# Kernel tuning notes

Hardware: AMD Instinct MI355X
Metric: run time of the kernel (lower is better)

The kernel has to match this reference:

```python
import jax, jax.numpy as jnp
import numpy as np

ALPHA = 1.702   # GLU sigmoid scale
LIMIT = 7.0     # clamp limit
K = 2           # experts per token


def setup_inputs() -> dict:
    key = jax.random.key(0)
    ks = jax.random.split(key, 4)
    B, S, H, E, I = 1, 1024, 1024, 8, 1024
    return {
        "hidden_states": jax.random.normal(ks[0], (B, S, H), jnp.float32),
        "router_weight": jax.random.normal(ks[1], (E, H), jnp.float32),
        "router_bias": jnp.zeros((E,), jnp.float32),
        "gate_up_proj": jax.random.normal(ks[2], (E, H, 2 * I), jnp.float32) * 0.02,
        "gate_up_bias": jnp.zeros((E, 2 * I), jnp.float32),
        "down_proj": jax.random.normal(ks[3], (E, I, H), jnp.float32) * 0.02,
        "down_bias": jnp.zeros((E, H), jnp.float32),
    }


def reference(hidden_states, router_weight, router_bias, gate_up_proj,
              gate_up_bias, down_proj, down_bias):
    B, S, H = hidden_states.shape
    E = router_weight.shape[0]
    I = down_proj.shape[1]
    T = B * S

    flat = hidden_states.reshape(T, H)

    # Router: softmax over experts, top-K selection (weights NOT renormalized).
    logits = flat @ router_weight.T + router_bias               # [T, E]
    scores = jax.nn.softmax(logits, axis=-1)
    topk_vals, topk_idx = jax.lax.top_k(scores, K)              # [T, K]

    # Dense per-token expert weight matrix (equivalent of dispatch metadata +
    # combine * topk_weights in the tt pipeline); top-k indices are unique.
    w = jnp.zeros((T, E), scores.dtype).at[
        jnp.arange(T)[:, None], topk_idx].set(topk_vals)        # [T, E]

    # Expert MLP with clamped GLU (gpt-oss style).
    gu = jnp.einsum('th,ehf->tef', flat, gate_up_proj) + gate_up_bias  # [T,E,2I]
    gate = jnp.minimum(gu[..., :I], LIMIT)
    up = jnp.clip(gu[..., I:], -LIMIT, LIMIT)
    glu = gate * jax.nn.sigmoid(gate * ALPHA)
    act = (up + 1.0) * glu                                       # [T, E, I]

    down = jnp.einsum('tei,eih->teh', act, down_proj) + down_bias  # [T, E, H]

    # Weighted combine over selected experts.
    out = jnp.einsum('teh,te->th', down, w)
    return out.reshape(B, S, H)
```

## Files before the change

kernel.cpp:

```cpp
#include <hip/hip_runtime.h>
#include <hip/hip_bf16.h>


typedef unsigned short u16;
typedef __attribute__((ext_vector_type(8))) __bf16 bf16x8;
typedef __attribute__((ext_vector_type(4))) float f32x4;
typedef __attribute__((ext_vector_type(16))) float f32x16;

#define T_TOK 1024
#define H_DIM 1024
#define E_NUM 8
#define I_DIM 1024
#define ALPHA 1.702f
#define LIMIT 7.0f

__device__ __forceinline__ u16 f2bf(float f) {
    unsigned u = __builtin_bit_cast(unsigned, f);
    u = (u + 0x7FFFu + ((u >> 16) & 1u)) >> 16;
    return (u16)u;
}

__device__ __forceinline__ unsigned pk2(float lo, float hi) {
#if defined(__has_builtin) && __has_builtin(__builtin_amdgcn_cvt_pk_bf16_f32)
    typedef __attribute__((ext_vector_type(2))) __bf16 bf16x2_t;
    bf16x2_t v = __builtin_amdgcn_cvt_pk_bf16_f32(lo, hi);
    return __builtin_bit_cast(unsigned, v);
#else
    return (unsigned)f2bf(lo) | ((unsigned)f2bf(hi) << 16);
#endif
}

__device__ __forceinline__ f32x16 mfma32(bf16x8 a, bf16x8 b, f32x16 c) {
    return __builtin_amdgcn_mfma_f32_32x32x16_bf16(a, b, c, 0, 0, 0);
}

__device__ __forceinline__ void gld16(const void* g, void* l) {
    __builtin_amdgcn_global_load_lds(
        (const __attribute__((address_space(1))) void*)g,
        (__attribute__((address_space(3))) void*)l, 16, 0, 0);
}

__device__ __forceinline__ void expert_range(const int* counts, int e,
                                             int& cnt, int& abase) {
    int a = 0, c = 0;
#pragma unroll
    for (int i = 0; i < E_NUM; ++i) {
        int v = counts[i];
        if (i < e) a += v;
        if (i == e) c = v;
    }
    cnt = c; abase = a;
}

__global__ __launch_bounds__(256) void k_cvt(
    const float* __restrict__ gup, const float* __restrict__ dp,
    u16* __restrict__ gupT, u16* __restrict__ dpT, int* __restrict__ counts)
{
    if (blockIdx.x == 0 && threadIdx.x < E_NUM) counts[threadIdx.x] = 0;
    const int b = blockIdx.x;
    const float* src; u16* dst; int C, k0, c0;
    if (b < 4096) {
        int e = b >> 9, t = b & 511;
        k0 = (t >> 5) * 64; c0 = (t & 31) * 64;
        src = gup + ((size_t)e << 21); dst = gupT + ((size_t)e << 21); C = 2048;
    } else {
        int b2 = b - 4096;
        int e = b2 >> 8, t = b2 & 255;
        k0 = (t >> 4) * 64; c0 = (t & 15) * 64;
        src = dp + ((size_t)e << 20); dst = dpT + ((size_t)e << 20); C = 1024;
    }
    __shared__ __align__(16) u16 Ls[64][72];
    const int tid = threadIdx.x;
    const int kq = tid >> 4, cq = tid & 15;
    float4 v0 = *(const float4*)(src + (size_t)(k0 + kq * 4 + 0) * C + c0 + cq * 4);
    float4 v1 = *(const float4*)(src + (size_t)(k0 + kq * 4 + 1) * C + c0 + cq * 4);
    float4 v2 = *(const float4*)(src + (size_t)(k0 + kq * 4 + 2) * C + c0 + cq * 4);
    float4 v3 = *(const float4*)(src + (size_t)(k0 + kq * 4 + 3) * C + c0 + cq * 4);
    const float* p0 = (const float*)&v0; const float* p1 = (const float*)&v1;
    const float* p2 = (const float*)&v2; const float* p3 = (const float*)&v3;
#pragma unroll
    for (int i = 0; i < 4; ++i) {
        *(uint2*)&Ls[cq * 4 + i][kq * 4] =
            make_uint2(pk2(p0[i], p1[i]), pk2(p2[i], p3[i]));
    }
    __syncthreads();
    const int oc = tid >> 2, och = (tid & 3) * 16;
    u16* orow = dst + (size_t)(c0 + oc) * 1024 + k0 + och;
    *(uint4*)(orow)     = *(uint4*)&Ls[oc][och];
    *(uint4*)(orow + 8) = *(uint4*)&Ls[oc][och + 8];
}

__global__ __launch_bounds__(256) void k_router(
    const float* __restrict__ x, const float* __restrict__ rw,
    const float* __restrict__ rb, const float* __restrict__ db,
    int* __restrict__ counts, int* __restrict__ tok_list,
    float* __restrict__ w_list, u16* __restrict__ xb,
    float* __restrict__ out)
{
    const int t = blockIdx.x;
    const int tid = threadIdx.x;
    const float4 xv = *(const float4*)(x + (size_t)t * H_DIM + tid * 4);

    *(uint2*)(xb + (size_t)t * H_DIM + tid * 4) =
        make_uint2(pk2(xv.x, xv.y), pk2(xv.z, xv.w));

    float p[E_NUM];
#pragma unroll
    for (int e = 0; e < E_NUM; ++e) {
        const float4 wv = *(const float4*)(rw + e * H_DIM + tid * 4);
        p[e] = xv.x * wv.x + xv.y * wv.y + xv.z * wv.z + xv.w * wv.w;
    }
#pragma unroll
    for (int off = 32; off; off >>= 1) {
#pragma unroll
        for (int e = 0; e < E_NUM; ++e) p[e] += __shfl_down(p[e], off, 64);
    }
    __shared__ float red[4][E_NUM];
    __shared__ int se[2];
    __shared__ float sw[2];
    const int lane = tid & 63, wvid = tid >> 6;
    if (lane == 0) {
#pragma unroll
        for (int e = 0; e < E_NUM; ++e) red[wvid][e] = p[e];
    }
    __syncthreads();
    if (tid == 0) {
        float lg[E_NUM];
#pragma unroll
        for (int e = 0; e < E_NUM; ++e)
            lg[e] = red[0][e] + red[1][e] + red[2][e] + red[3][e] + rb[e];
        float m1 = -1e30f, m2 = -1e30f; int i1 = 0, i2 = 0;
#pragma unroll
        for (int e = 0; e < E_NUM; ++e) {
            float l = lg[e];
            if (l > m1) { m2 = m1; i2 = i1; m1 = l; i1 = e; }
            else if (l > m2) { m2 = l; i2 = e; }
        }
        float s = 0.f;
#pragma unroll
        for (int e = 0; e < E_NUM; ++e) s += __expf(lg[e] - m1);
        const float w0 = 1.0f / s;
        const float w1 = __expf(m2 - m1) / s;
        int slot0 = atomicAdd(&counts[i1], 1);
        tok_list[i1 * T_TOK + slot0] = t;
        w_list[i1 * T_TOK + slot0] = w0;
        int slot1 = atomicAdd(&counts[i2], 1);
        tok_list[i2 * T_TOK + slot1] = t;
        w_list[i2 * T_TOK + slot1] = w1;
        se[0] = i1; se[1] = i2; sw[0] = w0; sw[1] = w1;
    }
    __syncthreads();
    const int e0 = se[0], e1 = se[1];
    const float w0 = sw[0], w1 = sw[1];
    const int c = tid * 4;
    float4 d0 = *(const float4*)(db + e0 * H_DIM + c);
    float4 d1 = *(const float4*)(db + e1 * H_DIM + c);
    float4 o;
    o.x = w0 * d0.x + w1 * d1.x;
    o.y = w0 * d0.y + w1 * d1.y;
    o.z = w0 * d0.z + w1 * d1.z;
    o.w = w0 * d0.w + w1 * d1.w;
    *(float4*)(out + (size_t)t * H_DIM + c) = o;
}

__global__ __launch_bounds__(256, 2) void k_gateup(
    const u16* __restrict__ gupT, const float* __restrict__ gub,
    const int* __restrict__ counts, const int* __restrict__ tok_list,
    const u16* __restrict__ xb, u16* __restrict__ act)
{
    const int e = blockIdx.z;
    int cnt, abase;
    expert_range(counts, e, cnt, abase);
    const int m0 = blockIdx.y * 128;
    if (m0 >= cnt) return;
    const int n0 = blockIdx.x * 64;
    const int tid = threadIdx.x;
    const int lane = tid & 63, wv = tid >> 6;
    const int wm = wv >> 1, wn = wv & 1;
    const int cl = lane & 31;
    const int kh = lane >> 5;

    __shared__ __align__(16) u16 As[3][128 * 32];
    __shared__ __align__(16) u16 Bs[3][128 * 32];

    const int lr = lane >> 2;
    const int lk = (((lane & 3) ^ (lr & 3)) << 3);
    const u16* gA[2];
    const u16* gB[2];
#pragma unroll
    for (int i = 0; i < 2; ++i) {
        int arow = wv * 32 + i * 16 + lr;
        int slot = m0 + arow;
        int tok = (slot < cnt) ? tok_list[e * T_TOK + slot] : 0;
        gA[i] = xb + (size_t)tok * H_DIM + lk;
        int brow = wv * 32 + i * 16 + lr;
        int col = (brow < 64) ? (n0 + brow) : (1024 + n0 + brow - 64);
        gB[i] = gupT + ((size_t)e << 21) + (size_t)col * 1024 + lk;
    }

    f32x16 accg[2], accu[2];
#pragma unroll
    for (int i = 0; i < 16; ++i) {
        accg[0][i] = 0.f; accg[1][i] = 0.f;
        accu[0][i] = 0.f; accu[1][i] = 0.f;
    }

#define GU_ST(BUF, KB)                                                         \
    {                                                                          \
        gld16(gA[0] + (KB), &As[BUF][(wv * 2 + 0) * 512]);                     \
        gld16(gA[1] + (KB), &As[BUF][(wv * 2 + 1) * 512]);                     \
        gld16(gB[0] + (KB), &Bs[BUF][(wv * 2 + 0) * 512]);                     \
        gld16(gB[1] + (KB), &Bs[BUF][(wv * 2 + 1) * 512]);                     \
    }
#define GU_MM(BUF)                                                             \
    {                                                                          \
        _Pragma("unroll")                                                      \
        for (int ks = 0; ks < 2; ++ks) {                                       \
            const int so = (((ks * 2 + kh) ^ (cl & 3)) << 3);                  \
            bf16x8 a0 = *(const bf16x8*)&As[BUF][(wm * 64 + cl) * 32 + so];      \
            bf16x8 a1 = *(const bf16x8*)&As[BUF][(wm * 64 + 32 + cl) * 32 + so]; \
            bf16x8 bg = *(const bf16x8*)&Bs[BUF][(wn * 32 + cl) * 32 + so];      \
            bf16x8 bu = *(const bf16x8*)&Bs[BUF][(64 + wn * 32 + cl) * 32 + so]; \
            accg[0] = mfma32(a0, bg, accg[0]);                                 \
            accu[0] = mfma32(a0, bu, accu[0]);                                 \
            accg[1] = mfma32(a1, bg, accg[1]);                                 \
            accu[1] = mfma32(a1, bu, accu[1]);                                 \
        }                                                                      \
    }

    GU_ST(0, 0);
    GU_ST(1, 32);
#pragma unroll
    for (int p = 0; p < 32; ++p) {
        if (p == 31) { asm volatile("s_waitcnt vmcnt(0) lgkmcnt(0)" ::: "memory"); }
        else         { asm volatile("s_waitcnt vmcnt(4) lgkmcnt(0)" ::: "memory"); }
        __builtin_amdgcn_s_barrier();
        if (p + 2 < 32) GU_ST((p + 2) % 3, (p + 2) * 32);
        GU_MM(p % 3);
    }
#undef GU_ST
#undef GU_MM

#pragma unroll
    for (int mf = 0; mf < 2; ++mf) {
#pragma unroll
        for (int r = 0; r < 16; ++r) {
            int row = wm * 64 + mf * 32 + (r & 3) + 8 * (r >> 2) + 4 * kh;
            int slot = m0 + row;
            if (slot >= cnt) continue;
            int col = n0 + wn * 32 + cl;
            float g = (mf == 0 ? accg[0][r] : accg[1][r]) + gub[e * 2048 + col];
            float u = (mf == 0 ? accu[0][r] : accu[1][r]) + gub[e * 2048 + 1024 + col];
            g = fminf(g, LIMIT);
            u = fminf(fmaxf(u, -LIMIT), LIMIT);
            float glu = g / (1.f + __expf(-ALPHA * g));
            act[(size_t)(abase + slot) * I_DIM + col] = f2bf((u + 1.f) * glu);
        }
    }
}

__global__ __launch_bounds__(256, 2) void k_down(
    const u16* __restrict__ dpT,
    const int* __restrict__ counts, const int* __restrict__ tok_list,
    const float* __restrict__ w_list,
    const u16* __restrict__ act, float* __restrict__ out)
{
    const int e = blockIdx.z;
    int cnt, abase;
    expert_range(counts, e, cnt, abase);
    const int m0 = blockIdx.y * 128;
    if (m0 >= cnt) return;
    const int n0 = blockIdx.x * 64;
    const int tid = threadIdx.x;
    const int lane = tid & 63, wv = tid >> 6;
    const int wm = wv >> 1, wn = wv & 1;
    const int cl = lane & 31, kh = lane >> 5;

    __shared__ __align__(16) u16 As[3][128 * 32];
    __shared__ __align__(16) u16 Bs[3][64 * 32];

    const int lr = lane >> 2;
    const int lk = (((lane & 3) ^ (lr & 3)) << 3);
    const u16* gA[2];
#pragma unroll
    for (int i = 0; i < 2; ++i) {
        int row = wv * 32 + i * 16 + lr;
        gA[i] = act + (size_t)(abase + m0 + row) * I_DIM + lk;
    }
    const u16* gBp;
    {
        int row = wv * 16 + lr;
        gBp = dpT + ((size_t)e << 20) + (size_t)(n0 + row) * 1024 + lk;
    }

    f32x16 acc0, acc1;
#pragma unroll
    for (int i = 0; i < 16; ++i) { acc0[i] = 0.f; acc1[i] = 0.f; }

#define DN_ST(BUF, KB)                                                         \
    {                                                                          \
        gld16(gA[0] + (KB), &As[BUF][(wv * 2 + 0) * 512]);                     \
        gld16(gA[1] + (KB), &As[BUF][(wv * 2 + 1) * 512]);                     \
        gld16(gBp + (KB), &Bs[BUF][wv * 512]);                                 \
    }
#define DN_MM(BUF)                                                             \
    {                                                                          \
        _Pragma("unroll")                                                      \
        for (int ks = 0; ks < 2; ++ks) {                                       \
            const int so = (((ks * 2 + kh) ^ (cl & 3)) << 3);                  \
            bf16x8 a0 = *(const bf16x8*)&As[BUF][(wm * 64 + cl) * 32 + so];      \
            bf16x8 a1 = *(const bf16x8*)&As[BUF][(wm * 64 + 32 + cl) * 32 + so]; \
            bf16x8 b  = *(const bf16x8*)&Bs[BUF][(wn * 32 + cl) * 32 + so];      \
            acc0 = mfma32(a0, b, acc0);                                        \
            acc1 = mfma32(a1, b, acc1);                                        \
        }                                                                      \
    }

    DN_ST(0, 0);
    DN_ST(1, 32);
#pragma unroll
    for (int p = 0; p < 32; ++p) {
        if (p == 31) { asm volatile("s_waitcnt vmcnt(0) lgkmcnt(0)" ::: "memory"); }
        else         { asm volatile("s_waitcnt vmcnt(3) lgkmcnt(0)" ::: "memory"); }
        __builtin_amdgcn_s_barrier();
        if (p + 2 < 32) DN_ST((p + 2) % 3, (p + 2) * 32);
        DN_MM(p % 3);
    }
#undef DN_ST
#undef DN_MM

#pragma unroll
    for (int mf = 0; mf < 2; ++mf) {
#pragma unroll
        for (int r = 0; r < 16; ++r) {
            int row = wm * 64 + mf * 32 + (r & 3) + 8 * (r >> 2) + 4 * kh;
            int slot = m0 + row;
            if (slot >= cnt) continue;
            float wgt = w_list[e * T_TOK + slot];
            int tok = tok_list[e * T_TOK + slot];
            int col = n0 + wn * 32 + cl;
            float v = (mf == 0 ? acc0[r] : acc1[r]) * wgt;
            atomicAdd(out + (size_t)tok * H_DIM + col, v);
        }
    }
}

extern "C" void kernel_launch(void* const* d_in, const int* in_sizes, int n_in,
                              void* d_out, int out_size, void* d_ws, size_t ws_size,
                              hipStream_t stream) {
    const float* x   = (const float*)d_in[0];
    const float* rw  = (const float*)d_in[1];
    const float* rb  = (const float*)d_in[2];
    const float* gup = (const float*)d_in[3];
    const float* gub = (const float*)d_in[4];
    const float* dp  = (const float*)d_in[5];
    const float* db  = (const float*)d_in[6];
    float* out = (float*)d_out;

    char* ws = (char*)d_ws;
    int*   counts   = (int*)(ws);
    int*   tok_list = (int*)(ws + 64);
    float* w_list   = (float*)(ws + 64 + 32768);
    u16*   xb       = (u16*)(ws + 65600);
    u16*   act      = (u16*)(ws + 65600 + 2097152);
    u16*   gupT     = (u16*)(ws + 8388608);
    u16*   dpT      = (u16*)(ws + 41943040);

    k_cvt<<<6144, 256, 0, stream>>>(gup, dp, gupT, dpT, counts);
    k_router<<<T_TOK, 256, 0, stream>>>(x, rw, rb, db, counts, tok_list, w_list,
                                        xb, out);
    k_gateup<<<dim3(16, 4, 8), 256, 0, stream>>>(gupT, gub, counts, tok_list,
                                                 xb, act);
    k_down<<<dim3(16, 4, 8), 256, 0, stream>>>(dpT, counts, tok_list, w_list,
                                               act, out);
}
```

Baseline: 238.2 us.

## Use 16x16 MFMA with smaller M tiles and split-K down projection

```diff
diff --git a/kernel.cpp b/kernel.cpp
--- a/kernel.cpp
+++ b/kernel.cpp
@@ -5,7 +5,6 @@
 typedef unsigned short u16;
 typedef __attribute__((ext_vector_type(8))) __bf16 bf16x8;
 typedef __attribute__((ext_vector_type(4))) float f32x4;
-typedef __attribute__((ext_vector_type(16))) float f32x16;
 
 #define T_TOK 1024
 #define H_DIM 1024
@@ -30,8 +29,8 @@
 #endif
 }
 
-__device__ __forceinline__ f32x16 mfma32(bf16x8 a, bf16x8 b, f32x16 c) {
-    return __builtin_amdgcn_mfma_f32_32x32x16_bf16(a, b, c, 0, 0, 0);
+__device__ __forceinline__ f32x4 mfma16(bf16x8 a, bf16x8 b, f32x4 c) {
+    return __builtin_amdgcn_mfma_f32_16x16x32_bf16(a, b, c, 0, 0, 0);
 }
 
 __device__ __forceinline__ void gld16(const void* g, void* l) {
@@ -163,7 +162,7 @@
     *(float4*)(out + (size_t)t * H_DIM + c) = o;
 }
 
-__global__ __launch_bounds__(256, 2) void k_gateup(
+__global__ __launch_bounds__(256, 4) void k_gateup(
     const u16* __restrict__ gupT, const float* __restrict__ gub,
     const int* __restrict__ counts, const int* __restrict__ tok_list,
     const u16* __restrict__ xb, u16* __restrict__ act)
@@ -171,61 +170,68 @@
     const int e = blockIdx.z;
     int cnt, abase;
     expert_range(counts, e, cnt, abase);
-    const int m0 = blockIdx.y * 128;
+    const int m0 = blockIdx.y * 64;
     if (m0 >= cnt) return;
     const int n0 = blockIdx.x * 64;
     const int tid = threadIdx.x;
     const int lane = tid & 63, wv = tid >> 6;
+    const int fm = lane & 15, kg = lane >> 4;
     const int wm = wv >> 1, wn = wv & 1;
-    const int cl = lane & 31;
-    const int kh = lane >> 5;
-
-    __shared__ __align__(16) u16 As[3][128 * 32];
+
+    __shared__ __align__(16) u16 As[3][64 * 32];
     __shared__ __align__(16) u16 Bs[3][128 * 32];
 
     const int lr = lane >> 2;
     const int lk = (((lane & 3) ^ (lr & 3)) << 3);
-    const u16* gA[2];
+    const u16* gA;
+    {
+        int row = wv * 16 + lr;
+        int slot = m0 + row;
+        int tok = (slot < cnt) ? tok_list[e * T_TOK + slot] : 0;
+        gA = xb + (size_t)tok * H_DIM + lk;
+    }
     const u16* gB[2];
 #pragma unroll
     for (int i = 0; i < 2; ++i) {
-        int arow = wv * 32 + i * 16 + lr;
-        int slot = m0 + arow;
-        int tok = (slot < cnt) ? tok_list[e * T_TOK + slot] : 0;
-        gA[i] = xb + (size_t)tok * H_DIM + lk;
-        int brow = wv * 32 + i * 16 + lr;
-        int col = (brow < 64) ? (n0 + brow) : (1024 + n0 + brow - 64);
+        int row = wv * 32 + i * 16 + lr;
+        int col = (row < 64) ? (n0 + row) : (1024 + n0 + row - 64);
         gB[i] = gupT + ((size_t)e << 21) + (size_t)col * 1024 + lk;
     }
 
-    f32x16 accg[2], accu[2];
-#pragma unroll
-    for (int i = 0; i < 16; ++i) {
-        accg[0][i] = 0.f; accg[1][i] = 0.f;
-        accu[0][i] = 0.f; accu[1][i] = 0.f;
-    }
+    f32x4 accg[2][2], accu[2][2];
+#pragma unroll
+    for (int m = 0; m < 2; ++m)
+#pragma unroll
+        for (int n = 0; n < 2; ++n) {
+            accg[m][n] = (f32x4){0.f, 0.f, 0.f, 0.f};
+            accu[m][n] = (f32x4){0.f, 0.f, 0.f, 0.f};
+        }
 
 #define GU_ST(BUF, KB)                                                         \
     {                                                                          \
-        gld16(gA[0] + (KB), &As[BUF][(wv * 2 + 0) * 512]);                     \
-        gld16(gA[1] + (KB), &As[BUF][(wv * 2 + 1) * 512]);                     \
+        gld16(gA + (KB), &As[BUF][wv * 512]);                                  \
         gld16(gB[0] + (KB), &Bs[BUF][(wv * 2 + 0) * 512]);                     \
         gld16(gB[1] + (KB), &Bs[BUF][(wv * 2 + 1) * 512]);                     \
     }
 #define GU_MM(BUF)                                                             \
     {                                                                          \
-        _Pragma("unroll")                                                      \
-        for (int ks = 0; ks < 2; ++ks) {                                       \
-            const int so = (((ks * 2 + kh) ^ (cl & 3)) << 3);                  \
-            bf16x8 a0 = *(const bf16x8*)&As[BUF][(wm * 64 + cl) * 32 + so];      \
-            bf16x8 a1 = *(const bf16x8*)&As[BUF][(wm * 64 + 32 + cl) * 32 + so]; \
-            bf16x8 bg = *(const bf16x8*)&Bs[BUF][(wn * 32 + cl) * 32 + so];      \
-            bf16x8 bu = *(const bf16x8*)&Bs[BUF][(64 + wn * 32 + cl) * 32 + so]; \
-            accg[0] = mfma32(a0, bg, accg[0]);                                 \
-            accu[0] = mfma32(a0, bu, accu[0]);                                 \
-            accg[1] = mfma32(a1, bg, accg[1]);                                 \
-            accu[1] = mfma32(a1, bu, accu[1]);                                 \
-        }                                                                      \
+        const int ko = ((kg ^ (fm & 3)) << 3);                                 \
+        bf16x8 a0 = *(const bf16x8*)&As[BUF][(wm * 32 + fm) * 32 + ko];        \
+        bf16x8 a1 = *(const bf16x8*)&As[BUF][(wm * 32 + 16 + fm) * 32 + ko];   \
+        bf16x8 bg0 = *(const bf16x8*)&Bs[BUF][(wn * 32 + fm) * 32 + ko];       \
+        bf16x8 bg1 = *(const bf16x8*)&Bs[BUF][(wn * 32 + 16 + fm) * 32 + ko];  \
+        bf16x8 bu0 = *(const bf16x8*)&Bs[BUF][(64 + wn * 32 + fm) * 32 + ko];  \
+        bf16x8 bu1 = *(const bf16x8*)&Bs[BUF][(64 + wn * 32 + 16 + fm) * 32 + ko]; \
+        __builtin_amdgcn_s_setprio(1);                                         \
+        accg[0][0] = mfma16(a0, bg0, accg[0][0]);                              \
+        accg[0][1] = mfma16(a0, bg1, accg[0][1]);                              \
+        accu[0][0] = mfma16(a0, bu0, accu[0][0]);                              \
+        accu[0][1] = mfma16(a0, bu1, accu[0][1]);                              \
+        accg[1][0] = mfma16(a1, bg0, accg[1][0]);                              \
+        accg[1][1] = mfma16(a1, bg1, accg[1][1]);                              \
+        accu[1][0] = mfma16(a1, bu0, accu[1][0]);                              \
+        accu[1][1] = mfma16(a1, bu1, accu[1][1]);                              \
+        __builtin_amdgcn_s_setprio(0);                                         \
     }
 
     GU_ST(0, 0);
@@ -233,7 +239,7 @@
 #pragma unroll
     for (int p = 0; p < 32; ++p) {
         if (p == 31) { asm volatile("s_waitcnt vmcnt(0) lgkmcnt(0)" ::: "memory"); }
-        else         { asm volatile("s_waitcnt vmcnt(4) lgkmcnt(0)" ::: "memory"); }
+        else         { asm volatile("s_waitcnt vmcnt(3) lgkmcnt(0)" ::: "memory"); }
         __builtin_amdgcn_s_barrier();
         if (p + 2 < 32) GU_ST((p + 2) % 3, (p + 2) * 32);
         GU_MM(p % 3);
@@ -242,105 +248,111 @@
 #undef GU_MM
 
 #pragma unroll
-    for (int mf = 0; mf < 2; ++mf) {
-#pragma unroll
-        for (int r = 0; r < 16; ++r) {
-            int row = wm * 64 + mf * 32 + (r & 3) + 8 * (r >> 2) + 4 * kh;
+    for (int m = 0; m < 2; ++m) {
+#pragma unroll
+        for (int r = 0; r < 4; ++r) {
+            int row = wm * 32 + m * 16 + kg * 4 + r;
             int slot = m0 + row;
             if (slot >= cnt) continue;
-            int col = n0 + wn * 32 + cl;
-            float g = (mf == 0 ? accg[0][r] : accg[1][r]) + gub[e * 2048 + col];
-            float u = (mf == 0 ? accu[0][r] : accu[1][r]) + gub[e * 2048 + 1024 + col];
-            g = fminf(g, LIMIT);
-            u = fminf(fmaxf(u, -LIMIT), LIMIT);
-            float glu = g / (1.f + __expf(-ALPHA * g));
-            act[(size_t)(abase + slot) * I_DIM + col] = f2bf((u + 1.f) * glu);
+            size_t arow = (size_t)(abase + slot) * I_DIM;
+#pragma unroll
+            for (int n = 0; n < 2; ++n) {
+                int cn = n0 + wn * 32 + n * 16 + fm;
+                float g = accg[m][n][r] + gub[e * 2048 + cn];
+                float u = accu[m][n][r] + gub[e * 2048 + 1024 + cn];
+                g = fminf(g, LIMIT);
+                u = fminf(fmaxf(u, -LIMIT), LIMIT);
+                float glu = g / (1.f + __expf(-ALPHA * g));
+                act[arow + cn] = f2bf((u + 1.f) * glu);
+            }
         }
     }
 }
 
-__global__ __launch_bounds__(256, 2) void k_down(
+__global__ __launch_bounds__(256, 4) void k_down(
     const u16* __restrict__ dpT,
     const int* __restrict__ counts, const int* __restrict__ tok_list,
     const float* __restrict__ w_list,
     const u16* __restrict__ act, float* __restrict__ out)
 {
-    const int e = blockIdx.z;
+    const int e = blockIdx.z & 7, ks = blockIdx.z >> 3;
     int cnt, abase;
     expert_range(counts, e, cnt, abase);
-    const int m0 = blockIdx.y * 128;
+    const int m0 = blockIdx.y * 64;
     if (m0 >= cnt) return;
     const int n0 = blockIdx.x * 64;
     const int tid = threadIdx.x;
     const int lane = tid & 63, wv = tid >> 6;
+    const int fm = lane & 15, kg = lane >> 4;
     const int wm = wv >> 1, wn = wv & 1;
-    const int cl = lane & 31, kh = lane >> 5;
-
-    __shared__ __align__(16) u16 As[3][128 * 32];
+
+    __shared__ __align__(16) u16 As[3][64 * 32];
     __shared__ __align__(16) u16 Bs[3][64 * 32];
 
     const int lr = lane >> 2;
     const int lk = (((lane & 3) ^ (lr & 3)) << 3);
-    const u16* gA[2];
-#pragma unroll
-    for (int i = 0; i < 2; ++i) {
-        int row = wv * 32 + i * 16 + lr;
-        gA[i] = act + (size_t)(abase + m0 + row) * I_DIM + lk;
-    }
-    const u16* gBp;
+    const u16* gA;
+    const u16* gB;
     {
         int row = wv * 16 + lr;
-        gBp = dpT + ((size_t)e << 20) + (size_t)(n0 + row) * 1024 + lk;
-    }
-
-    f32x16 acc0, acc1;
-#pragma unroll
-    for (int i = 0; i < 16; ++i) { acc0[i] = 0.f; acc1[i] = 0.f; }
+        gA = act + (size_t)(abase + m0 + row) * I_DIM + ks * 512 + lk;
+        gB = dpT + ((size_t)e << 20) + (size_t)(n0 + row) * 1024 + ks * 512 + lk;
+    }
+
+    f32x4 acc[2][2];
+#pragma unroll
+    for (int m = 0; m < 2; ++m)
+#pragma unroll
+        for (int n = 0; n < 2; ++n) acc[m][n] = (f32x4){0.f, 0.f, 0.f, 0.f};
 
 #define DN_ST(BUF, KB)                                                         \
     {                                                                          \
-        gld16(gA[0] + (KB), &As[BUF][(wv * 2 + 0) * 512]);                     \
-        gld16(gA[1] + (KB), &As[BUF][(wv * 2 + 1) * 512]);                     \
-        gld16(gBp + (KB), &Bs[BUF][wv * 512]);                                 \
+        gld16(gA + (KB), &As[BUF][wv * 512]);                                  \
+        gld16(gB + (KB), &Bs[BUF][wv * 512]);                                  \
     }
 #define DN_MM(BUF)                                                             \
     {                                                                          \
-        _Pragma("unroll")                                                      \
-        for (int ks = 0; ks < 2; ++ks) {                                       \
-            const int so = (((ks * 2 + kh) ^ (cl & 3)) << 3);                  \
-            bf16x8 a0 = *(const bf16x8*)&As[BUF][(wm * 64 + cl) * 32 + so];      \
-            bf16x8 a1 = *(const bf16x8*)&As[BUF][(wm * 64 + 32 + cl) * 32 + so]; \
-            bf16x8 b  = *(const bf16x8*)&Bs[BUF][(wn * 32 + cl) * 32 + so];      \
-            acc0 = mfma32(a0, b, acc0);                                        \
-            acc1 = mfma32(a1, b, acc1);                                        \
-        }                                                                      \
+        const int ko = ((kg ^ (fm & 3)) << 3);                                 \
+        bf16x8 a0 = *(const bf16x8*)&As[BUF][(wm * 32 + fm) * 32 + ko];        \
+        bf16x8 a1 = *(const bf16x8*)&As[BUF][(wm * 32 + 16 + fm) * 32 + ko];   \
+        bf16x8 b0 = *(const bf16x8*)&Bs[BUF][(wn * 32 + fm) * 32 + ko];        \
+        bf16x8 b1 = *(const bf16x8*)&Bs[BUF][(wn * 32 + 16 + fm) * 32 + ko];   \
+        __builtin_amdgcn_s_setprio(1);                                         \
+        acc[0][0] = mfma16(a0, b0, acc[0][0]);                                 \
+        acc[0][1] = mfma16(a0, b1, acc[0][1]);                                 \
+        acc[1][0] = mfma16(a1, b0, acc[1][0]);                                 \
+        acc[1][1] = mfma16(a1, b1, acc[1][1]);                                 \
+        __builtin_amdgcn_s_setprio(0);                                         \
     }
 
     DN_ST(0, 0);
     DN_ST(1, 32);
 #pragma unroll
-    for (int p = 0; p < 32; ++p) {
-        if (p == 31) { asm volatile("s_waitcnt vmcnt(0) lgkmcnt(0)" ::: "memory"); }
-        else         { asm volatile("s_waitcnt vmcnt(3) lgkmcnt(0)" ::: "memory"); }
+    for (int p = 0; p < 16; ++p) {
+        if (p == 15) { asm volatile("s_waitcnt vmcnt(0) lgkmcnt(0)" ::: "memory"); }
+        else         { asm volatile("s_waitcnt vmcnt(2) lgkmcnt(0)" ::: "memory"); }
         __builtin_amdgcn_s_barrier();
-        if (p + 2 < 32) DN_ST((p + 2) % 3, (p + 2) * 32);
+        if (p + 2 < 16) DN_ST((p + 2) % 3, (p + 2) * 32);
         DN_MM(p % 3);
     }
 #undef DN_ST
 #undef DN_MM
 
 #pragma unroll
-    for (int mf = 0; mf < 2; ++mf) {
-#pragma unroll
-        for (int r = 0; r < 16; ++r) {
-            int row = wm * 64 + mf * 32 + (r & 3) + 8 * (r >> 2) + 4 * kh;
+    for (int m = 0; m < 2; ++m) {
+#pragma unroll
+        for (int r = 0; r < 4; ++r) {
+            int row = wm * 32 + m * 16 + kg * 4 + r;
             int slot = m0 + row;
             if (slot >= cnt) continue;
             float wgt = w_list[e * T_TOK + slot];
             int tok = tok_list[e * T_TOK + slot];
-            int col = n0 + wn * 32 + cl;
-            float v = (mf == 0 ? acc0[r] : acc1[r]) * wgt;
-            atomicAdd(out + (size_t)tok * H_DIM + col, v);
+            float* orow = out + (size_t)tok * H_DIM;
+#pragma unroll
+            for (int n = 0; n < 2; ++n) {
+                int col = n0 + wn * 32 + n * 16 + fm;
+                atomicAdd(orow + col, acc[m][n][r] * wgt);
+            }
         }
     }
 }
@@ -369,8 +381,8 @@
     k_cvt<<<6144, 256, 0, stream>>>(gup, dp, gupT, dpT, counts);
     k_router<<<T_TOK, 256, 0, stream>>>(x, rw, rb, db, counts, tok_list, w_list,
                                         xb, out);
-    k_gateup<<<dim3(16, 4, 8), 256, 0, stream>>>(gupT, gub, counts, tok_list,
-                                                 xb, act);
-    k_down<<<dim3(16, 4, 8), 256, 0, stream>>>(dpT, counts, tok_list, w_list,
-                                               act, out);
-}
+    k_gateup<<<dim3(16, 16, 8), 256, 0, stream>>>(gupT, gub, counts, tok_list,
+                                                  xb, act);
+    k_down<<<dim3(16, 16, 16), 256, 0, stream>>>(dpT, counts, tok_list, w_list,
+                                                 act, out);
+}
```

New measurement: 220.1 us. -7.6%, faster.
